# Kernel optimization log

Measured on AMD Instinct MI355X. Metric: run time of the kernel, lower is better.

Reference implementation:

```python
import jax, jax.numpy as jnp
import numpy as np

S, B, V, E, H, L = 500, 64, 50257, 512, 512, 2


def setup_inputs() -> dict:
    key = jax.random.key(0)
    ks = jax.random.split(key, 12)
    u = lambda k, shape, s: jax.random.uniform(k, shape, jnp.float32, -s, s)
    kstd = 1.0 / np.sqrt(H)
    return {
        "inputs": jax.random.randint(ks[0], (S, B), 0, V, dtype=jnp.int64),
        "text_lengths": jax.random.randint(ks[1], (B,), 1, S, dtype=jnp.int64),
        "embedding": jax.random.normal(ks[2], (V, E), jnp.float32),
        "W_ih": u(ks[3], (4 * H, E), kstd),   # PyTorch LSTM gate order: i,f,g,o
        "W_hh": u(ks[4], (4 * H, H), kstd),
        "b_ih": u(ks[5], (4 * H,), kstd),
        "b_hh": u(ks[6], (4 * H,), kstd),
        "W_word": u(ks[7], (H, H), 0.1),
        "b_word": jnp.zeros((H, 1), jnp.float32),
        "w_proj": u(ks[8], (H, 1), 0.1),
        "dec_W": u(ks[9], (L, H), kstd),
        "dec_b": u(ks[10], (L,), kstd),
    }


def _lstm(x, W_ih, W_hh, b_ih, b_hh):
    # x: [S, B, E] -> states [S, B, H]
    Bsz = x.shape[1]
    Hn = W_hh.shape[1]
    # precompute input projections for all timesteps in one GEMM
    xproj = jnp.einsum('sbe,ge->sbg', x, W_ih) + b_ih + b_hh  # [S, B, 4H]

    def step(carry, xp):
        h, c = carry
        z = xp + h @ W_hh.T  # [B, 4H]
        i, f, g, o = jnp.split(z, 4, axis=-1)
        i, f, o = jax.nn.sigmoid(i), jax.nn.sigmoid(f), jax.nn.sigmoid(o)
        c = f * c + i * jnp.tanh(g)
        h = o * jnp.tanh(c)
        return (h, c), h

    h0 = jnp.zeros((Bsz, Hn), x.dtype)
    _, hs = jax.lax.scan(step, (h0, h0), xproj)
    return hs  # [S, B, H]


def reference(inputs, text_lengths, embedding, W_ih, W_hh, b_ih, b_hh,
              W_word, b_word, w_proj, dec_W, dec_b):
    # eval mode: dropout is identity
    embedded = embedding[inputs]                       # [S, B, E]
    states = _lstm(embedded, W_ih, W_hh, b_ih, b_hh)   # [S, B, H]
    # batch_matmul_bias with tanh: tanh(states @ W_word + b_word^T)
    word_squish = jnp.tanh(jnp.einsum('sbh,hk->sbk', states, W_word) + b_word[:, 0])
    # batch_matmul: project to scalar score per (s, b)
    word_attn = jnp.einsum('sbh,hk->sbk', word_squish, w_proj)[..., 0]  # [S, B]
    # softmax over sequence dim (nn.Softmax on [B, S] -> dim=1)
    attn = jax.nn.softmax(word_attn.T, axis=1).T       # [S, B]
    # attention_mul: weighted sum over S, keepdim -> [1, B, H]
    pooled = jnp.einsum('sb,sbh->bh', attn, states)[None]
    return pooled @ dec_W.T + dec_b                    # [1, B, labels]
```

## Files before the change

kernel.cpp:

```cpp
#include <hip/hip_runtime.h>


#define S_LEN 500
#define BATCH 64
#define EDIM 512
#define HDIM 512
#define TEAMS 8
#define WGS_PER_TEAM 32
#define TB 8
#define NBLOCKS (TEAMS * WGS_PER_TEAM)
#define NTHREADS 512
#define NSLICE 8
#define SLICE_LEN 63

typedef unsigned long long ull;
typedef __attribute__((ext_vector_type(8))) short short8v;
typedef __attribute__((ext_vector_type(4))) float float4v;
typedef __attribute__((ext_vector_type(4))) unsigned int uint4v;

#define XPROJ_BYTES  ((size_t)S_LEN * 2048 * BATCH * 4)
#define STATES_OFF   XPROJ_BYTES
#define STATES_BYTES ((size_t)S_LEN * BATCH * HDIM * 4)
#define HBUF_OFF     (STATES_OFF + STATES_BYTES)
#define HBUF_BYTES   ((size_t)2 * TEAMS * TB * HDIM * 8)
#define PART_OFF     (HBUF_OFF + HBUF_BYTES)
#define PART_BYTES   (4 * S_LEN * BATCH * 4)
#define POOLP_OFF    (PART_OFF + PART_BYTES)
#define POOLP_BYTES  ((size_t)BATCH * NSLICE * HDIM * 4)
#define ML_OFF       (POOLP_OFF + POOLP_BYTES)
#define ML_BYTES     (BATCH * NSLICE * 2 * 4)

__global__ __launch_bounds__(256) void xproj_gemm(
    const int* __restrict__ idx, const float* __restrict__ emb,
    const float* __restrict__ W_ih, const float* __restrict__ b_ih,
    const float* __restrict__ b_hh, float* __restrict__ xproj) {
  __shared__ float At[16][132];
  __shared__ float Bt[16][132];
  __shared__ int sidx[128];

  const int tid = threadIdx.x;
  const int sb0 = blockIdx.x * 128;
  const int g0  = blockIdx.y * 128;
  if (tid < 128) sidx[tid] = idx[sb0 + tid];

  const int ty = tid >> 4, tx = tid & 15;
  const int ra = tid & 127, pp = tid >> 7;

  float acc[8][8];
#pragma unroll
  for (int i = 0; i < 8; ++i)
#pragma unroll
    for (int j = 0; j < 8; ++j) acc[i][j] = 0.f;

  __syncthreads();

  for (int k0 = 0; k0 < 512; k0 += 16) {
    const float* pa = &W_ih[(size_t)(g0 + ra) * 512 + k0 + 8 * pp];
    float4 a0 = *(const float4*)pa, a1 = *(const float4*)(pa + 4);
    const float* pb = &emb[(size_t)sidx[ra] * 512 + k0 + 8 * pp];
    float4 b0 = *(const float4*)pb, b1 = *(const float4*)(pb + 4);
    At[8*pp+0][ra]=a0.x; At[8*pp+1][ra]=a0.y; At[8*pp+2][ra]=a0.z; At[8*pp+3][ra]=a0.w;
    At[8*pp+4][ra]=a1.x; At[8*pp+5][ra]=a1.y; At[8*pp+6][ra]=a1.z; At[8*pp+7][ra]=a1.w;
    Bt[8*pp+0][ra]=b0.x; Bt[8*pp+1][ra]=b0.y; Bt[8*pp+2][ra]=b0.z; Bt[8*pp+3][ra]=b0.w;
    Bt[8*pp+4][ra]=b1.x; Bt[8*pp+5][ra]=b1.y; Bt[8*pp+6][ra]=b1.z; Bt[8*pp+7][ra]=b1.w;
    __syncthreads();
#pragma unroll
    for (int kk = 0; kk < 16; ++kk) {
      float4 x0 = *(const float4*)&At[kk][ty * 8];
      float4 x1 = *(const float4*)&At[kk][ty * 8 + 4];
      float4 y0 = *(const float4*)&Bt[kk][tx * 8];
      float4 y1 = *(const float4*)&Bt[kk][tx * 8 + 4];
      float av[8] = {x0.x, x0.y, x0.z, x0.w, x1.x, x1.y, x1.z, x1.w};
      float bv[8] = {y0.x, y0.y, y0.z, y0.w, y1.x, y1.y, y1.z, y1.w};
#pragma unroll
      for (int i = 0; i < 8; ++i)
#pragma unroll
        for (int j = 0; j < 8; ++j) acc[i][j] = fmaf(av[i], bv[j], acc[i][j]);
    }
    __syncthreads();
  }
  const int sbb = sb0 + tx * 8;
  const int s  = sbb >> 6;
  const int tm = (sbb & 63) >> 3;
#pragma unroll
  for (int i = 0; i < 8; ++i) {
    const int g = g0 + ty * 8 + i;
    const float bias = b_ih[g] + b_hh[g];
    float* dst = &xproj[(((size_t)s * TEAMS + tm) * 2048 + g) * 8];
    float4 v0 = {acc[i][0] + bias, acc[i][1] + bias, acc[i][2] + bias, acc[i][3] + bias};
    float4 v1 = {acc[i][4] + bias, acc[i][5] + bias, acc[i][6] + bias, acc[i][7] + bias};
    *(float4*)dst = v0;
    *(float4*)(dst + 4) = v1;
  }
}

__global__ __launch_bounds__(NTHREADS, 1) void lstm_persistent(
    const float* __restrict__ xproj, const float* __restrict__ W_hh,
    float* __restrict__ states, ull* __restrict__ h_buf) {
  __shared__ float red[2][8][4][16][5];
  __shared__ unsigned hT[8][4][66];

  const int team = blockIdx.x & 7;
  const int wg   = blockIdx.x >> 3;
  const int tid  = threadIdx.x;
  const int wv   = tid >> 6;
  const int l    = tid & 63;

  const int col = l & 15;
  const int kg  = l >> 4;

  short8v Ahi[4][2], Alo[4][2];
#pragma unroll
  for (int j = 0; j < 4; ++j)
#pragma unroll
    for (int ks = 0; ks < 2; ++ks) {
      const float* wr = &W_hh[((size_t)(16 * wg + col) + 512 * j) * 512
                              + 64 * wv + 32 * ks + 8 * kg];
      unsigned hw[4], lw[4];
#pragma unroll
      for (int p = 0; p < 4; ++p) {
        float w0 = wr[2 * p], w1 = wr[2 * p + 1];
        unsigned u0 = __float_as_uint(w0), u1 = __float_as_uint(w1);
        hw[p] = (u1 & 0xffff0000u) | (u0 >> 16);
        float l0 = w0 - __uint_as_float(u0 & 0xffff0000u);
        float l1 = w1 - __uint_as_float(u1 & 0xffff0000u);
        lw[p] = (__float_as_uint(l1) & 0xffff0000u) | (__float_as_uint(l0) >> 16);
      }
      uint4v ph = {hw[0], hw[1], hw[2], hw[3]};
      uint4v pl = {lw[0], lw[1], lw[2], lw[3]};
      Ahi[j][ks] = __builtin_bit_cast(short8v, ph);
      Alo[j][ks] = __builtin_bit_cast(short8v, pl);
    }

  const int gu = l & 15, gbl = l >> 4;
  const int unit = 16 * wg + gu;
  float c_state = 0.f;
  const float* xpbase = xproj + (size_t)(16 * wg + gu) * 8 + (wv * 4 + gbl);

  const bool bact = (col < 4);

  for (int s = 0; s < S_LEN; ++s) {
    const int par = s & 1, par2 = (s + 1) & 1;

    ull pre0 = 0, pre1 = 0, pre2 = 0, pre3 = 0;
    ull pre4 = 0, pre5 = 0, pre6 = 0, pre7 = 0;
    const ull* hb0 = h_buf + (((size_t)par * TEAMS + team) * TB) * HDIM
                     + (size_t)64 * wv + l;
    if (s > 0) {
      pre0 = __hip_atomic_load(hb0 + 0 * HDIM, __ATOMIC_RELAXED, __HIP_MEMORY_SCOPE_AGENT);
      pre1 = __hip_atomic_load(hb0 + 1 * HDIM, __ATOMIC_RELAXED, __HIP_MEMORY_SCOPE_AGENT);
      pre2 = __hip_atomic_load(hb0 + 2 * HDIM, __ATOMIC_RELAXED, __HIP_MEMORY_SCOPE_AGENT);
      pre3 = __hip_atomic_load(hb0 + 3 * HDIM, __ATOMIC_RELAXED, __HIP_MEMORY_SCOPE_AGENT);
      pre4 = __hip_atomic_load(hb0 + 4 * HDIM, __ATOMIC_RELAXED, __HIP_MEMORY_SCOPE_AGENT);
      pre5 = __hip_atomic_load(hb0 + 5 * HDIM, __ATOMIC_RELAXED, __HIP_MEMORY_SCOPE_AGENT);
      pre6 = __hip_atomic_load(hb0 + 6 * HDIM, __ATOMIC_RELAXED, __HIP_MEMORY_SCOPE_AGENT);
      pre7 = __hip_atomic_load(hb0 + 7 * HDIM, __ATOMIC_RELAXED, __HIP_MEMORY_SCOPE_AGENT);
    }

#pragma unroll
    for (int G = 0; G < 2; ++G) {
      float xv0, xv1, xv2, xv3;
      if (wv == G) {
        const float* p = xpbase + ((size_t)s * TEAMS + team) * (2048 * 8);
        xv0 = p[0]; xv1 = p[512 * 8]; xv2 = p[1024 * 8]; xv3 = p[1536 * 8];
      }

      float4v acc[4];
#pragma unroll
      for (int j = 0; j < 4; ++j) acc[j] = (float4v){0.f, 0.f, 0.f, 0.f};

      if (s > 0) {
        ull r0 = (G == 0) ? pre0 : pre4;
        ull r1 = (G == 0) ? pre1 : pre5;
        ull r2 = (G == 0) ? pre2 : pre6;
        ull r3 = (G == 0) ? pre3 : pre7;
        bool ok = ((int)(r0 >> 32) == s) & ((int)(r1 >> 32) == s) &
                  ((int)(r2 >> 32) == s) & ((int)(r3 >> 32) == s);
        if (!__all(ok)) {
          const ull* hb = hb0 + (size_t)(G * 4) * HDIM;
          int spins = 0;
          for (;;) {
            r0 = __hip_atomic_load(hb + 0 * HDIM, __ATOMIC_RELAXED, __HIP_MEMORY_SCOPE_AGENT);
            r1 = __hip_atomic_load(hb + 1 * HDIM, __ATOMIC_RELAXED, __HIP_MEMORY_SCOPE_AGENT);
            r2 = __hip_atomic_load(hb + 2 * HDIM, __ATOMIC_RELAXED, __HIP_MEMORY_SCOPE_AGENT);
            r3 = __hip_atomic_load(hb + 3 * HDIM, __ATOMIC_RELAXED, __HIP_MEMORY_SCOPE_AGENT);
            ok = ((int)(r0 >> 32) == s) & ((int)(r1 >> 32) == s) &
                 ((int)(r2 >> 32) == s) & ((int)(r3 >> 32) == s);
            if (__all(ok)) break;
            __builtin_amdgcn_s_sleep(1);
            if (++spins > (1 << 18)) break;
          }
        }
        hT[wv][0][l] = (unsigned)r0;
        hT[wv][1][l] = (unsigned)r1;
        hT[wv][2][l] = (unsigned)r2;
        hT[wv][3][l] = (unsigned)r3;

        short8v Bhi[2], Blo[2];
#pragma unroll
        for (int ks = 0; ks < 2; ++ks) {
          unsigned hw[4], lw[4];
#pragma unroll
          for (int p = 0; p < 4; ++p) {
            unsigned u0 = 0, u1 = 0;
            if (bact) {
              const uint2 v = *(const uint2*)&hT[wv][col][32 * ks + 8 * kg + 2 * p];
              u0 = v.x; u1 = v.y;
            }
            hw[p] = (u1 & 0xffff0000u) | (u0 >> 16);
            lw[p] = (u1 << 16) | (u0 & 0xffffu);
          }
          uint4v ph = {hw[0], hw[1], hw[2], hw[3]};
          uint4v pl = {lw[0], lw[1], lw[2], lw[3]};
          Bhi[ks] = __builtin_bit_cast(short8v, ph);
          Blo[ks] = __builtin_bit_cast(short8v, pl);
        }
#pragma unroll
        for (int j = 0; j < 4; ++j) {
#pragma unroll
          for (int ks = 0; ks < 2; ++ks) {
            acc[j] = __builtin_amdgcn_mfma_f32_16x16x32_bf16(Ahi[j][ks], Bhi[ks], acc[j], 0, 0, 0);
            acc[j] = __builtin_amdgcn_mfma_f32_16x16x32_bf16(Alo[j][ks], Bhi[ks], acc[j], 0, 0, 0);
            acc[j] = __builtin_amdgcn_mfma_f32_16x16x32_bf16(Ahi[j][ks], Blo[ks], acc[j], 0, 0, 0);
          }
        }
      }

      if (bact) {
#pragma unroll
        for (int j = 0; j < 4; ++j)
#pragma unroll
          for (int r = 0; r < 4; ++r)
            red[G][wv][j][kg * 4 + r][col] = acc[j][r];
      }
      __syncthreads();

      if (wv == G) {
        float z0 = xv0, z1 = xv1, z2 = xv2, z3 = xv3;
#pragma unroll
        for (int w2 = 0; w2 < 8; ++w2) {
          z0 += red[G][w2][0][gu][gbl];
          z1 += red[G][w2][1][gu][gbl];
          z2 += red[G][w2][2][gu][gbl];
          z3 += red[G][w2][3][gu][gbl];
        }
        float i_ = 1.f / (1.f + expf(-z0));
        float f_ = 1.f / (1.f + expf(-z1));
        float g_ = tanhf(z2);
        float o_ = 1.f / (1.f + expf(-z3));
        c_state = f_ * c_state + i_ * g_;
        float h_ = o_ * tanhf(c_state);
        unsigned uh = __float_as_uint(h_);
        unsigned hi16 = uh >> 16;
        float rem = h_ - __uint_as_float(uh & 0xffff0000u);
        unsigned lo16 = __float_as_uint(rem) >> 16;
        ull pv = ((ull)(unsigned)(s + 1) << 32) | (ull)((hi16 << 16) | lo16);
        __hip_atomic_store(
            &h_buf[(((size_t)par2 * TEAMS + team) * TB + G * 4 + gbl) * HDIM + unit],
            pv, __ATOMIC_RELAXED, __HIP_MEMORY_SCOPE_AGENT);
        states[((size_t)s * BATCH + team * TB + G * 4 + gbl) * HDIM + unit] = h_;
      }
    }
  }
}

#define ATP 132
__global__ __launch_bounds__(256) void attn_gemm(
    const float* __restrict__ states, const float* __restrict__ W_word,
    const float* __restrict__ b_word, const float* __restrict__ w_proj,
    float* __restrict__ part) {
  __shared__ float At[16][ATP];
  __shared__ float Bt[16][ATP];
  __shared__ float redl[128][17];

  const int tid = threadIdx.x;
  const int m0 = blockIdx.x * 128;
  const int n0 = blockIdx.y * 128;
  const int ty = tid >> 4, tx = tid & 15;

  float acc[8][8];
#pragma unroll
  for (int i = 0; i < 8; ++i)
#pragma unroll
    for (int j = 0; j < 8; ++j) acc[i][j] = 0.f;

  for (int k0 = 0; k0 < 512; k0 += 16) {
#pragma unroll
    for (int it = 0; it < 2; ++it) {
      int m = (tid >> 2) + 64 * it;
      int kq = tid & 3;
      float4 v = *(const float4*)&states[(size_t)(m0 + m) * 512 + k0 + 4 * kq];
      At[4 * kq + 0][m] = v.x; At[4 * kq + 1][m] = v.y;
      At[4 * kq + 2][m] = v.z; At[4 * kq + 3][m] = v.w;
    }
#pragma unroll
    for (int it = 0; it < 2; ++it) {
      int kr = (tid >> 5) + 8 * it;
      int nq = tid & 31;
      float4 v = *(const float4*)&W_word[(size_t)(k0 + kr) * 512 + n0 + 4 * nq];
      *(float4*)&Bt[kr][4 * nq] = v;
    }
    __syncthreads();
#pragma unroll
    for (int kk = 0; kk < 16; ++kk) {
      float4 a0 = *(const float4*)&At[kk][ty * 8];
      float4 a1 = *(const float4*)&At[kk][ty * 8 + 4];
      float4 b0 = *(const float4*)&Bt[kk][tx * 8];
      float4 b1 = *(const float4*)&Bt[kk][tx * 8 + 4];
      float av[8] = {a0.x, a0.y, a0.z, a0.w, a1.x, a1.y, a1.z, a1.w};
      float bv[8] = {b0.x, b0.y, b0.z, b0.w, b1.x, b1.y, b1.z, b1.w};
#pragma unroll
      for (int i = 0; i < 8; ++i)
#pragma unroll
        for (int j = 0; j < 8; ++j) acc[i][j] = fmaf(av[i], bv[j], acc[i][j]);
    }
    __syncthreads();
  }
  float bw[8], wp[8];
  {
    float4 v0 = *(const float4*)&b_word[n0 + tx * 8];
    float4 v1 = *(const float4*)&b_word[n0 + tx * 8 + 4];
    bw[0]=v0.x; bw[1]=v0.y; bw[2]=v0.z; bw[3]=v0.w; bw[4]=v1.x; bw[5]=v1.y; bw[6]=v1.z; bw[7]=v1.w;
    float4 u0 = *(const float4*)&w_proj[n0 + tx * 8];
    float4 u1 = *(const float4*)&w_proj[n0 + tx * 8 + 4];
    wp[0]=u0.x; wp[1]=u0.y; wp[2]=u0.z; wp[3]=u0.w; wp[4]=u1.x; wp[5]=u1.y; wp[6]=u1.z; wp[7]=u1.w;
  }
#pragma unroll
  for (int i = 0; i < 8; ++i) {
    float rs = 0.f;
#pragma unroll
    for (int j = 0; j < 8; ++j) rs += tanhf(acc[i][j] + bw[j]) * wp[j];
    redl[ty * 8 + i][tx] = rs;
  }
  __syncthreads();
  if (tid < 128) {
    float ssum = 0.f;
#pragma unroll
    for (int x = 0; x < 16; ++x) ssum += redl[tid][x];
    part[(size_t)blockIdx.y * (S_LEN * BATCH) + m0 + tid] = ssum;
  }
}

__global__ __launch_bounds__(256) void pool_partial(
    const float* __restrict__ part, const float* __restrict__ states,
    float* __restrict__ poolP, float* __restrict__ ml) {
  const int b = blockIdx.x >> 3;
  const int sl = blockIdx.x & 7;
  const int s0 = sl * SLICE_LEN;
  const int len = (sl == 7) ? (S_LEN - 7 * SLICE_LEN) : SLICE_LEN;
  const int tid = threadIdx.x;

  __shared__ float es[SLICE_LEN];
  __shared__ float redm[256];

  float sc = -1e30f;
  if (tid < len) {
    const int t = (s0 + tid) * BATCH + b;
    sc = part[t] + part[S_LEN * BATCH + t] + part[2 * S_LEN * BATCH + t] +
         part[3 * S_LEN * BATCH + t];
  }
  redm[tid] = sc;
  __syncthreads();
  for (int o = 128; o > 0; o >>= 1) {
    if (tid < o) redm[tid] = fmaxf(redm[tid], redm[tid + o]);
    __syncthreads();
  }
  const float m_sl = redm[0];
  __syncthreads();
  float e = 0.f;
  if (tid < len) e = expf(sc - m_sl);
  if (tid < SLICE_LEN) es[tid] = (tid < len) ? e : 0.f;
  redm[tid] = e;
  __syncthreads();
  for (int o = 128; o > 0; o >>= 1) {
    if (tid < o) redm[tid] += redm[tid + o];
    __syncthreads();
  }
  if (tid == 0) {
    ml[(b * NSLICE + sl) * 2 + 0] = m_sl;
    ml[(b * NSLICE + sl) * 2 + 1] = redm[0];
  }
  __syncthreads();

  for (int h = tid; h < HDIM; h += 256) {
    float a = 0.f;
    for (int s = 0; s < len; ++s)
      a = fmaf(es[s], states[((size_t)(s0 + s) * BATCH + b) * HDIM + h], a);
    poolP[((size_t)b * NSLICE + sl) * HDIM + h] = a;
  }
}

__global__ __launch_bounds__(256) void pool_merge_decode(
    const float* __restrict__ poolP, const float* __restrict__ ml,
    const float* __restrict__ dec_W, const float* __restrict__ dec_b,
    float* __restrict__ out) {
  const int b = blockIdx.x;
  const int tid = threadIdx.x;
  __shared__ float pool[HDIM];
  __shared__ float redm[256];
  __shared__ float wsl[NSLICE];

  if (tid == 0) {
    float gmax = -1e30f;
#pragma unroll
    for (int i = 0; i < NSLICE; ++i) gmax = fmaxf(gmax, ml[(b * NSLICE + i) * 2]);
    float Z = 0.f;
#pragma unroll
    for (int i = 0; i < NSLICE; ++i) {
      float w = expf(ml[(b * NSLICE + i) * 2] - gmax);
      wsl[i] = w;
      Z = fmaf(ml[(b * NSLICE + i) * 2 + 1], w, Z);
    }
    redm[0] = 1.f / Z;
  }
  __syncthreads();
  const float inv = redm[0];

  for (int h = tid; h < HDIM; h += 256) {
    float a = 0.f;
#pragma unroll
    for (int i = 0; i < NSLICE; ++i)
      a = fmaf(wsl[i], poolP[((size_t)b * NSLICE + i) * HDIM + h], a);
    pool[h] = a * inv;
  }
  __syncthreads();
  const int lcls = tid >> 7, ch = tid & 127;
  float p = 0.f;
#pragma unroll
  for (int j = 0; j < 4; ++j)
    p = fmaf(pool[ch * 4 + j], dec_W[lcls * HDIM + ch * 4 + j], p);
  redm[tid] = p;
  __syncthreads();
  for (int o = 64; o > 0; o >>= 1) {
    if (ch < o) redm[tid] += redm[tid + o];
    __syncthreads();
  }
  if (ch == 0) out[b * 2 + lcls] = redm[tid] + dec_b[lcls];
}

extern "C" void kernel_launch(void* const* d_in, const int* in_sizes, int n_in,
                              void* d_out, int out_size, void* d_ws, size_t ws_size,
                              hipStream_t stream) {
  const int*   idx    = (const int*)d_in[0];
  const float* emb    = (const float*)d_in[2];
  const float* W_ih   = (const float*)d_in[3];
  const float* W_hh   = (const float*)d_in[4];
  const float* b_ih   = (const float*)d_in[5];
  const float* b_hh   = (const float*)d_in[6];
  const float* W_word = (const float*)d_in[7];
  const float* b_word = (const float*)d_in[8];
  const float* w_proj = (const float*)d_in[9];
  const float* dec_W  = (const float*)d_in[10];
  const float* dec_b  = (const float*)d_in[11];
  float* out = (float*)d_out;

  char* ws = (char*)d_ws;
  float* xproj  = (float*)ws;
  float* states = (float*)(ws + STATES_OFF);
  ull*   h_buf  = (ull*)(ws + HBUF_OFF);
  float* part   = (float*)(ws + PART_OFF);
  float* poolP  = (float*)(ws + POOLP_OFF);
  float* ml     = (float*)(ws + ML_OFF);

  hipMemsetAsync(h_buf, 0, HBUF_BYTES, stream);

  xproj_gemm<<<dim3(250, 16), 256, 0, stream>>>(idx, emb, W_ih, b_ih, b_hh, xproj);

  void* args[] = {(void*)&xproj, (void*)&W_hh, (void*)&states, (void*)&h_buf};
  hipLaunchCooperativeKernel(lstm_persistent, dim3(NBLOCKS), dim3(NTHREADS), args, 0, stream);

  attn_gemm<<<dim3(250, 4), 256, 0, stream>>>(states, W_word, b_word, w_proj, part);
  pool_partial<<<BATCH * NSLICE, 256, 0, stream>>>(part, states, poolP, ml);
  pool_merge_decode<<<BATCH, 256, 0, stream>>>(poolP, ml, dec_W, dec_b, out);
}
```

Before: 2.824 ms.

## Process all eight batch rows per LSTM step in one MFMA pass

The recurrent step previously split the team's 8 batch rows into two groups of 4, each with its own wait, MFMA pass and block barrier, and half of each B tile was zero. Now each step waits once for all 8 h rows, fills 8 columns of the B operand, runs one MFMA pass and one barrier, and 128 threads do the gate math. This halves the per-step barriers and MFMA work. The trade-off is that the first group can no longer start computing while the second group's h is still arriving, and the reduction buffer alternates by step parity to avoid a second barrier.

Measured after the change: 3.000 ms. 1.06x slower.

```diff
diff --git a/kernel.cpp b/kernel.cpp
--- a/kernel.cpp
+++ b/kernel.cpp
@@ -97,8 +97,8 @@
 __global__ __launch_bounds__(NTHREADS, 1) void lstm_persistent(
     const float* __restrict__ xproj, const float* __restrict__ W_hh,
     float* __restrict__ states, ull* __restrict__ h_buf) {
-  __shared__ float red[2][8][4][16][5];
-  __shared__ unsigned hT[8][4][66];
+  __shared__ float red[2][8][4][16][9];
+  __shared__ unsigned hT[8][8][66];
 
   const int team = blockIdx.x & 7;
   const int wg   = blockIdx.x >> 3;
@@ -132,134 +132,120 @@
       Alo[j][ks] = __builtin_bit_cast(short8v, pl);
     }
 
-  const int gu = l & 15, gbl = l >> 4;
+  const int gu = tid & 15, gb = (tid >> 4) & 7;
   const int unit = 16 * wg + gu;
   float c_state = 0.f;
-  const float* xpbase = xproj + (size_t)(16 * wg + gu) * 8 + (wv * 4 + gbl);
-
-  const bool bact = (col < 4);
+  const float* xpbase = xproj + (size_t)(16 * wg + gu) * 8 + gb;
+
+  const bool bact = (col < 8);
 
   for (int s = 0; s < S_LEN; ++s) {
     const int par = s & 1, par2 = (s + 1) & 1;
 
-    ull pre0 = 0, pre1 = 0, pre2 = 0, pre3 = 0;
-    ull pre4 = 0, pre5 = 0, pre6 = 0, pre7 = 0;
-    const ull* hb0 = h_buf + (((size_t)par * TEAMS + team) * TB) * HDIM
-                     + (size_t)64 * wv + l;
+    float xv0, xv1, xv2, xv3;
+    if (tid < 128) {
+      const float* p = xpbase + ((size_t)s * TEAMS + team) * (2048 * 8);
+      xv0 = p[0]; xv1 = p[512 * 8]; xv2 = p[1024 * 8]; xv3 = p[1536 * 8];
+    }
+
+    float4v acc[4];
+#pragma unroll
+    for (int j = 0; j < 4; ++j) acc[j] = (float4v){0.f, 0.f, 0.f, 0.f};
+
     if (s > 0) {
-      pre0 = __hip_atomic_load(hb0 + 0 * HDIM, __ATOMIC_RELAXED, __HIP_MEMORY_SCOPE_AGENT);
-      pre1 = __hip_atomic_load(hb0 + 1 * HDIM, __ATOMIC_RELAXED, __HIP_MEMORY_SCOPE_AGENT);
-      pre2 = __hip_atomic_load(hb0 + 2 * HDIM, __ATOMIC_RELAXED, __HIP_MEMORY_SCOPE_AGENT);
-      pre3 = __hip_atomic_load(hb0 + 3 * HDIM, __ATOMIC_RELAXED, __HIP_MEMORY_SCOPE_AGENT);
-      pre4 = __hip_atomic_load(hb0 + 4 * HDIM, __ATOMIC_RELAXED, __HIP_MEMORY_SCOPE_AGENT);
-      pre5 = __hip_atomic_load(hb0 + 5 * HDIM, __ATOMIC_RELAXED, __HIP_MEMORY_SCOPE_AGENT);
-      pre6 = __hip_atomic_load(hb0 + 6 * HDIM, __ATOMIC_RELAXED, __HIP_MEMORY_SCOPE_AGENT);
-      pre7 = __hip_atomic_load(hb0 + 7 * HDIM, __ATOMIC_RELAXED, __HIP_MEMORY_SCOPE_AGENT);
-    }
-
-#pragma unroll
-    for (int G = 0; G < 2; ++G) {
-      float xv0, xv1, xv2, xv3;
-      if (wv == G) {
-        const float* p = xpbase + ((size_t)s * TEAMS + team) * (2048 * 8);
-        xv0 = p[0]; xv1 = p[512 * 8]; xv2 = p[1024 * 8]; xv3 = p[1536 * 8];
+      const ull* hb0 = h_buf + (((size_t)par * TEAMS + team) * TB) * HDIM
+                       + (size_t)64 * wv + l;
+      ull r0, r1, r2, r3, r4, r5, r6, r7;
+      int spins = 0;
+      for (;;) {
+        r0 = __hip_atomic_load(hb0 + 0 * HDIM, __ATOMIC_RELAXED, __HIP_MEMORY_SCOPE_AGENT);
+        r1 = __hip_atomic_load(hb0 + 1 * HDIM, __ATOMIC_RELAXED, __HIP_MEMORY_SCOPE_AGENT);
+        r2 = __hip_atomic_load(hb0 + 2 * HDIM, __ATOMIC_RELAXED, __HIP_MEMORY_SCOPE_AGENT);
+        r3 = __hip_atomic_load(hb0 + 3 * HDIM, __ATOMIC_RELAXED, __HIP_MEMORY_SCOPE_AGENT);
+        r4 = __hip_atomic_load(hb0 + 4 * HDIM, __ATOMIC_RELAXED, __HIP_MEMORY_SCOPE_AGENT);
+        r5 = __hip_atomic_load(hb0 + 5 * HDIM, __ATOMIC_RELAXED, __HIP_MEMORY_SCOPE_AGENT);
+        r6 = __hip_atomic_load(hb0 + 6 * HDIM, __ATOMIC_RELAXED, __HIP_MEMORY_SCOPE_AGENT);
+        r7 = __hip_atomic_load(hb0 + 7 * HDIM, __ATOMIC_RELAXED, __HIP_MEMORY_SCOPE_AGENT);
+        bool ok = ((int)(r0 >> 32) == s) & ((int)(r1 >> 32) == s) &
+                  ((int)(r2 >> 32) == s) & ((int)(r3 >> 32) == s) &
+                  ((int)(r4 >> 32) == s) & ((int)(r5 >> 32) == s) &
+                  ((int)(r6 >> 32) == s) & ((int)(r7 >> 32) == s);
+        if (__all(ok)) break;
+        __builtin_amdgcn_s_sleep(1);
+        if (++spins > (1 << 18)) break;
       }
-
-      float4v acc[4];
-#pragma unroll
-      for (int j = 0; j < 4; ++j) acc[j] = (float4v){0.f, 0.f, 0.f, 0.f};
-
-      if (s > 0) {
-        ull r0 = (G == 0) ? pre0 : pre4;
-        ull r1 = (G == 0) ? pre1 : pre5;
-        ull r2 = (G == 0) ? pre2 : pre6;
-        ull r3 = (G == 0) ? pre3 : pre7;
-        bool ok = ((int)(r0 >> 32) == s) & ((int)(r1 >> 32) == s) &
-                  ((int)(r2 >> 32) == s) & ((int)(r3 >> 32) == s);
-        if (!__all(ok)) {
-          const ull* hb = hb0 + (size_t)(G * 4) * HDIM;
-          int spins = 0;
-          for (;;) {
-            r0 = __hip_atomic_load(hb + 0 * HDIM, __ATOMIC_RELAXED, __HIP_MEMORY_SCOPE_AGENT);
-            r1 = __hip_atomic_load(hb + 1 * HDIM, __ATOMIC_RELAXED, __HIP_MEMORY_SCOPE_AGENT);
-            r2 = __hip_atomic_load(hb + 2 * HDIM, __ATOMIC_RELAXED, __HIP_MEMORY_SCOPE_AGENT);
-            r3 = __hip_atomic_load(hb + 3 * HDIM, __ATOMIC_RELAXED, __HIP_MEMORY_SCOPE_AGENT);
-            ok = ((int)(r0 >> 32) == s) & ((int)(r1 >> 32) == s) &
-                 ((int)(r2 >> 32) == s) & ((int)(r3 >> 32) == s);
-            if (__all(ok)) break;
-            __builtin_amdgcn_s_sleep(1);
-            if (++spins > (1 << 18)) break;
+      hT[wv][0][l] = (unsigned)r0;
+      hT[wv][1][l] = (unsigned)r1;
+      hT[wv][2][l] = (unsigned)r2;
+      hT[wv][3][l] = (unsigned)r3;
+      hT[wv][4][l] = (unsigned)r4;
+      hT[wv][5][l] = (unsigned)r5;
+      hT[wv][6][l] = (unsigned)r6;
+      hT[wv][7][l] = (unsigned)r7;
+
+      short8v Bhi[2], Blo[2];
+#pragma unroll
+      for (int ks = 0; ks < 2; ++ks) {
+        unsigned hw[4], lw[4];
+#pragma unroll
+        for (int p = 0; p < 4; ++p) {
+          unsigned u0 = 0, u1 = 0;
+          if (bact) {
+            const uint2 v = *(const uint2*)&hT[wv][col][32 * ks + 8 * kg + 2 * p];
+            u0 = v.x; u1 = v.y;
           }
+          hw[p] = (u1 & 0xffff0000u) | (u0 >> 16);
+          lw[p] = (u1 << 16) | (u0 & 0xffffu);
         }
-        hT[wv][0][l] = (unsigned)r0;
-        hT[wv][1][l] = (unsigned)r1;
-        hT[wv][2][l] = (unsigned)r2;
-        hT[wv][3][l] = (unsigned)r3;
-
-        short8v Bhi[2], Blo[2];
+        uint4v ph = {hw[0], hw[1], hw[2], hw[3]};
+        uint4v pl = {lw[0], lw[1], lw[2], lw[3]};
+        Bhi[ks] = __builtin_bit_cast(short8v, ph);
+        Blo[ks] = __builtin_bit_cast(short8v, pl);
+      }
+#pragma unroll
+      for (int j = 0; j < 4; ++j) {
 #pragma unroll
         for (int ks = 0; ks < 2; ++ks) {
-          unsigned hw[4], lw[4];
-#pragma unroll
-          for (int p = 0; p < 4; ++p) {
-            unsigned u0 = 0, u1 = 0;
-            if (bact) {
-              const uint2 v = *(const uint2*)&hT[wv][col][32 * ks + 8 * kg + 2 * p];
-              u0 = v.x; u1 = v.y;
-            }
-            hw[p] = (u1 & 0xffff0000u) | (u0 >> 16);
-            lw[p] = (u1 << 16) | (u0 & 0xffffu);
-          }
-          uint4v ph = {hw[0], hw[1], hw[2], hw[3]};
-          uint4v pl = {lw[0], lw[1], lw[2], lw[3]};
-          Bhi[ks] = __builtin_bit_cast(short8v, ph);
-          Blo[ks] = __builtin_bit_cast(short8v, pl);
-        }
-#pragma unroll
-        for (int j = 0; j < 4; ++j) {
-#pragma unroll
-          for (int ks = 0; ks < 2; ++ks) {
-            acc[j] = __builtin_amdgcn_mfma_f32_16x16x32_bf16(Ahi[j][ks], Bhi[ks], acc[j], 0, 0, 0);
-            acc[j] = __builtin_amdgcn_mfma_f32_16x16x32_bf16(Alo[j][ks], Bhi[ks], acc[j], 0, 0, 0);
-            acc[j] = __builtin_amdgcn_mfma_f32_16x16x32_bf16(Ahi[j][ks], Blo[ks], acc[j], 0, 0, 0);
-          }
+          acc[j] = __builtin_amdgcn_mfma_f32_16x16x32_bf16(Ahi[j][ks], Bhi[ks], acc[j], 0, 0, 0);
+          acc[j] = __builtin_amdgcn_mfma_f32_16x16x32_bf16(Alo[j][ks], Bhi[ks], acc[j], 0, 0, 0);
+          acc[j] = __builtin_amdgcn_mfma_f32_16x16x32_bf16(Ahi[j][ks], Blo[ks], acc[j], 0, 0, 0);
         }
       }
-
-      if (bact) {
-#pragma unroll
-        for (int j = 0; j < 4; ++j)
-#pragma unroll
-          for (int r = 0; r < 4; ++r)
-            red[G][wv][j][kg * 4 + r][col] = acc[j][r];
+    }
+
+    if (bact) {
+#pragma unroll
+      for (int j = 0; j < 4; ++j)
+#pragma unroll
+        for (int r = 0; r < 4; ++r)
+          red[par][wv][j][kg * 4 + r][col] = acc[j][r];
+    }
+    __syncthreads();
+
+    if (tid < 128) {
+      float z0 = xv0, z1 = xv1, z2 = xv2, z3 = xv3;
+#pragma unroll
+      for (int w2 = 0; w2 < 8; ++w2) {
+        z0 += red[par][w2][0][gu][gb];
+        z1 += red[par][w2][1][gu][gb];
+        z2 += red[par][w2][2][gu][gb];
+        z3 += red[par][w2][3][gu][gb];
       }
-      __syncthreads();
-
-      if (wv == G) {
-        float z0 = xv0, z1 = xv1, z2 = xv2, z3 = xv3;
-#pragma unroll
-        for (int w2 = 0; w2 < 8; ++w2) {
-          z0 += red[G][w2][0][gu][gbl];
-          z1 += red[G][w2][1][gu][gbl];
-          z2 += red[G][w2][2][gu][gbl];
-          z3 += red[G][w2][3][gu][gbl];
-        }
-        float i_ = 1.f / (1.f + expf(-z0));
-        float f_ = 1.f / (1.f + expf(-z1));
-        float g_ = tanhf(z2);
-        float o_ = 1.f / (1.f + expf(-z3));
-        c_state = f_ * c_state + i_ * g_;
-        float h_ = o_ * tanhf(c_state);
-        unsigned uh = __float_as_uint(h_);
-        unsigned hi16 = uh >> 16;
-        float rem = h_ - __uint_as_float(uh & 0xffff0000u);
-        unsigned lo16 = __float_as_uint(rem) >> 16;
-        ull pv = ((ull)(unsigned)(s + 1) << 32) | (ull)((hi16 << 16) | lo16);
-        __hip_atomic_store(
-            &h_buf[(((size_t)par2 * TEAMS + team) * TB + G * 4 + gbl) * HDIM + unit],
-            pv, __ATOMIC_RELAXED, __HIP_MEMORY_SCOPE_AGENT);
-        states[((size_t)s * BATCH + team * TB + G * 4 + gbl) * HDIM + unit] = h_;
-      }
+      float i_ = 1.f / (1.f + expf(-z0));
+      float f_ = 1.f / (1.f + expf(-z1));
+      float g_ = tanhf(z2);
+      float o_ = 1.f / (1.f + expf(-z3));
+      c_state = f_ * c_state + i_ * g_;
+      float h_ = o_ * tanhf(c_state);
+      unsigned uh = __float_as_uint(h_);
+      unsigned hi16 = uh >> 16;
+      float rem = h_ - __uint_as_float(uh & 0xffff0000u);
+      unsigned lo16 = __float_as_uint(rem) >> 16;
+      ull pv = ((ull)(unsigned)(s + 1) << 32) | (ull)((hi16 << 16) | lo16);
+      __hip_atomic_store(
+          &h_buf[(((size_t)par2 * TEAMS + team) * TB + gb) * HDIM + unit],
+          pv, __ATOMIC_RELAXED, __HIP_MEMORY_SCOPE_AGENT);
+      states[((size_t)s * BATCH + team * TB + gb) * HDIM + unit] = h_;
     }
   }
 }
```
